# Kernel tuning notes

Hardware: AMD Instinct MI355X
Metric: run time of the kernel (lower is better)

## Reference

```python
import jax, jax.numpy as jnp
import numpy as np
import math

B, D, NH, HD, FF, P, IMG = 4, 768, 12, 64, 3072, 16, 256
L = (IMG // P) ** 2      # 256 tokens
PD = P * P * 3           # 768 patch dim
GRID = IMG // P          # 16


def setup_inputs() -> dict:
    key = jax.random.key(0)
    ks = iter(jax.random.split(key, 80))
    def nrm(shape, s=0.02):
        return jax.random.normal(next(ks), shape, jnp.float32) * s
    return {
        "x": jax.random.normal(next(ks), (B, 3, IMG, IMG), jnp.float32),
        "pe_norm_w": jnp.ones((PD,), jnp.float32),
        "pe_proj_w": nrm((PD, D)),
        "pe_proj_b": jnp.zeros((D,), jnp.float32),
        "pe_norm_out_w": jnp.ones((D,), jnp.float32),
        "pos_embed": nrm((1, L, D)),
        "in_attn_norm_w": jnp.ones((6, D), jnp.float32),
        "in_qkv_w": nrm((6, D, 3 * D)),
        "in_out_w": nrm((6, D, D)),
        "in_ff_norm_w": jnp.ones((6, D), jnp.float32),
        "in_w1": nrm((6, D, 2 * FF)),
        "in_w2": nrm((6, FF, D)),
        "mid_attn_norm_w": jnp.ones((3, D), jnp.float32),
        "mid_qkv_w": nrm((3, D, 3 * D)),
        "mid_out_w": nrm((3, D, D)),
        "mid_ff_norm_w": jnp.ones((3, D), jnp.float32),
        "mid_w1": nrm((3, D, 2 * FF)),
        "mid_w2": nrm((3, FF, D)),
        "out_skip_w": nrm((2 * D, D)),
        "out_skip_b": jnp.zeros((D,), jnp.float32),
        "out_attn_norm_w": jnp.ones((D,), jnp.float32),
        "out_qkv_w": nrm((D, 3 * D)),
        "out_out_w": nrm((D, D)),
        "out_ff_norm_w": jnp.ones((D,), jnp.float32),
        "out_w1": nrm((D, 2 * FF)),
        "out_w2": nrm((FF, D)),
        "final_norm_w": jnp.ones((D,), jnp.float32),
        "ol_proj_w": nrm((D, PD)),
        "ol_proj_b": jnp.zeros((PD,), jnp.float32),
        "rb_conv_in_w": nrm((128, 3, 3, 3), 0.1),
        "rb_gn_w": jnp.ones((5, 128), jnp.float32),
        "rb_gn_b": jnp.zeros((5, 128), jnp.float32),
        "rb_conv1_w": nrm((128, 1, 5, 5), 0.1),
        "rb_conv2_w": nrm((128, 1, 5, 5), 0.1),
        "head_conv_w": nrm((1, 128, 3, 3), 0.1),
    }


def _mish(x):
    return x * jnp.tanh(jax.nn.softplus(x))


def _rms(x, w, eps=1e-5):
    return x * jax.lax.rsqrt(jnp.mean(x * x, axis=-1, keepdims=True) + eps) * w


def _attn(x, qkv_w, out_w):
    b, l, _ = x.shape
    q, k, v = jnp.split(x @ qkv_w, 3, axis=-1)
    s = 1.0 / math.sqrt(HD)  # applied to BOTH q and k, as in source
    q = (q * s).reshape(b, l, NH, HD)
    k = (k * s).reshape(b, l, NH, HD)
    v = v.reshape(b, l, NH, HD)
    logits = jnp.einsum('bqhd,bkhd->bhqk', q, k).astype(jnp.float32)
    w = jax.nn.softmax(logits, axis=-1).astype(x.dtype)
    o = jnp.einsum('bhqk,bkhd->bqhd', w, v).reshape(b, l, NH * HD)
    return o @ out_w


def _ff(x, w1, w2):
    a, g = jnp.split(x @ w1, 2, axis=-1)
    return (_mish(a) * g) @ w2


def _block(x, an, qkv, ow, fn, w1, w2):
    x = x + _attn(_rms(x, an), qkv, ow)
    x = x + _ff(_rms(x, fn), w1, w2)
    return x


def _gn(x, w, b, groups=8, eps=1e-5):
    bb, c, h, ww = x.shape
    xg = x.reshape(bb, groups, c // groups, h, ww)
    m = jnp.mean(xg, axis=(2, 3, 4), keepdims=True)
    v = jnp.var(xg, axis=(2, 3, 4), keepdims=True)
    xn = ((xg - m) * jax.lax.rsqrt(v + eps)).reshape(bb, c, h, ww)
    return xn * w[:, None, None] + b[:, None, None]


def _conv(x, w, pad, dil=1, groups=1):
    xp = jnp.pad(x, ((0, 0), (0, 0), (pad, pad), (pad, pad)), mode='reflect')
    return jax.lax.conv_general_dilated(
        xp, w, window_strides=(1, 1), padding='VALID', rhs_dilation=(dil, dil),
        feature_group_count=groups, dimension_numbers=('NCHW', 'OIHW', 'NCHW'))


def _forward(x, pe_norm_w, pe_proj_w, pe_proj_b, pe_norm_out_w, pos_embed,
             in_attn_norm_w, in_qkv_w, in_out_w, in_ff_norm_w, in_w1, in_w2,
             mid_attn_norm_w, mid_qkv_w, mid_out_w, mid_ff_norm_w, mid_w1, mid_w2,
             out_skip_w, out_skip_b, out_attn_norm_w, out_qkv_w, out_out_w,
             out_ff_norm_w, out_w1, out_w2, final_norm_w, ol_proj_w, ol_proj_b,
             rb_conv_in_w, rb_gn_w, rb_gn_b, rb_conv1_w, rb_conv2_w, head_conv_w):
    b = x.shape[0]
    # PatchEmbed: b c (h p1) (w p2) -> b (h w) (p1 p2 c)
    t = x.reshape(b, 3, GRID, P, GRID, P).transpose(0, 2, 4, 3, 5, 1).reshape(b, L, PD)
    t = _rms(t, pe_norm_w)
    t = t @ pe_proj_w + pe_proj_b
    t = _rms(t, pe_norm_out_w)
    t = t + pos_embed
    # U-ViT trunk: 6 in blocks (skips saved), 3 middle, 1 out block (source typo -> single out block)
    skips = []
    for i in range(6):
        t = _block(t, in_attn_norm_w[i], in_qkv_w[i], in_out_w[i],
                   in_ff_norm_w[i], in_w1[i], in_w2[i])
        skips.append(t)
    for i in range(3):
        t = _block(t, mid_attn_norm_w[i], mid_qkv_w[i], mid_out_w[i],
                   mid_ff_norm_w[i], mid_w1[i], mid_w2[i])
    t = jnp.concatenate([t, skips[-1]], axis=-1) @ out_skip_w + out_skip_b
    t = _block(t, out_attn_norm_w, out_qkv_w, out_out_w, out_ff_norm_w, out_w1, out_w2)
    t = _rms(t, final_norm_w)
    # OutBlock: proj, dropout(eval=identity), unpatchify to b 3 256 256
    t = t @ ol_proj_w + ol_proj_b
    img = t.reshape(b, GRID, GRID, P, P, 3).transpose(0, 5, 1, 3, 2, 4).reshape(b, 3, IMG, IMG)
    # ResNetBlock(128)
    h = _conv(img, rb_conv_in_w, 1)
    h = _mish(_gn(h, rb_gn_w[0], rb_gn_b[0]))
    res = h
    h = _mish(_gn(_conv(h, rb_conv1_w, 2, 1, 128), rb_gn_w[1], rb_gn_b[1]))
    h = res + h
    h = _mish(_gn(h, rb_gn_w[2], rb_gn_b[2]))
    res = h
    h = _mish(_gn(_conv(h, rb_conv2_w, 6, 3, 128), rb_gn_w[3], rb_gn_b[3]))
    h = res + h
    h = _mish(_gn(h, rb_gn_w[4], rb_gn_b[4]))
    return _conv(h, head_conv_w, 1)  # [B, 1, 256, 256]


def reference(x, pe_norm_w, pe_proj_w, pe_proj_b, pe_norm_out_w, pos_embed,
              in_attn_norm_w, in_qkv_w, in_out_w, in_ff_norm_w, in_w1, in_w2,
              mid_attn_norm_w, mid_qkv_w, mid_out_w, mid_ff_norm_w, mid_w1, mid_w2,
              out_skip_w, out_skip_b, out_attn_norm_w, out_qkv_w, out_out_w,
              out_ff_norm_w, out_w1, out_w2, final_norm_w, ol_proj_w, ol_proj_b,
              rb_conv_in_w, rb_gn_w, rb_gn_b, rb_conv1_w, rb_conv2_w, head_conv_w):
    return _forward(x, pe_norm_w, pe_proj_w, pe_proj_b, pe_norm_out_w, pos_embed,
                    in_attn_norm_w, in_qkv_w, in_out_w, in_ff_norm_w, in_w1, in_w2,
                    mid_attn_norm_w, mid_qkv_w, mid_out_w, mid_ff_norm_w, mid_w1, mid_w2,
                    out_skip_w, out_skip_b, out_attn_norm_w, out_qkv_w, out_out_w,
                    out_ff_norm_w, out_w1, out_w2, final_norm_w, ol_proj_w, ol_proj_b,
                    rb_conv_in_w, rb_gn_w, rb_gn_b, rb_conv1_w, rb_conv2_w, head_conv_w)
```

## Files before the change

### kernel.cpp

```cpp
#include <hip/hip_runtime.h>
#include <math.h>

#define B_ 4
#define D_ 768
#define NH_ 12
#define HD_ 64
#define FF_ 3072
#define L_ 256
#define PD_ 768
#define GRID_ 16
#define P_ 16
#define IMG_ 256
#define M_ (B_*L_)
#define NCONV_ (B_*128*IMG_*IMG_)

typedef __attribute__((ext_vector_type(8))) short short8;
typedef __attribute__((ext_vector_type(4))) float f32x4;
typedef __attribute__((ext_vector_type(4))) unsigned short us4;
typedef __attribute__((ext_vector_type(8))) unsigned short us8;
typedef unsigned short ushort_t;

__device__ __forceinline__ float mishf(float x){
    float e = __expf(x);
    float u = (1.f + e) * (1.f + e);
    return x * (1.f - 2.f / (u + 1.f));
}

__device__ __forceinline__ int refl(int i, int n){
    if (i < 0) i = -i;
    if (i >= n) i = 2*n - 2 - i;
    return i;
}

__device__ __forceinline__ ushort_t f2bf(float f){
    unsigned int u = __float_as_uint(f);
    unsigned int r = (u + 0x7FFFu + ((u >> 16) & 1u)) >> 16;
    return (ushort_t)r;
}
__device__ __forceinline__ float bf2f(ushort_t u){
    return __uint_as_float(((unsigned int)u) << 16);
}

__device__ __forceinline__ void block_red2(float& s, float& q){
    #pragma unroll
    for (int o = 32; o > 0; o >>= 1){ s += __shfl_down(s, o); q += __shfl_down(q, o); }
    __shared__ float r1[4], r2[4];
    int tid = threadIdx.x;
    if ((tid & 63) == 0){ r1[tid>>6] = s; r2[tid>>6] = q; }
    __syncthreads();
    if (tid == 0){ s = r1[0]+r1[1]+r1[2]+r1[3]; q = r2[0]+r2[1]+r2[2]+r2[3]; }
    __syncthreads();
}

__global__ __launch_bounds__(256) void k_patchify(const float* __restrict__ x, float* __restrict__ t){
    int idx = blockIdx.x*256 + threadIdx.x;
    int d = idx % PD_; int l = (idx/PD_) % L_; int b = idx/(PD_*L_);
    int c = d % 3; int p = d / 3; int p1 = p / P_; int p2 = p % P_;
    int gh = l / GRID_; int gw = l % GRID_;
    int sy = gh*P_ + p1, sx = gw*P_ + p2;
    t[idx] = x[(((size_t)b*3 + c)*IMG_ + sy)*IMG_ + sx];
}

__global__ __launch_bounds__(256) void k_wt(const float* __restrict__ b0, const float* __restrict__ b1,
                                            const float* __restrict__ b2, int n0, int n1,
                                            ushort_t* __restrict__ dst, int K, int N){
    int z = blockIdx.z;
    size_t sz = (size_t)K * N;
    const float* src = (z < n0) ? b0 + (size_t)z*sz
                     : (z < n0+n1) ? b1 + (size_t)(z-n0)*sz
                     : b2 + (size_t)(z-n0-n1)*sz;
    ushort_t* out = dst + (size_t)z*sz;
    __shared__ float ld[32][33];
    int k0 = blockIdx.y*32, nc0 = blockIdx.x*32;
    int tid = threadIdx.x;
    int c = tid & 31, r8 = tid >> 5;
    #pragma unroll
    for (int i = 0; i < 4; ++i){
        int k = r8 + i*8;
        ld[k][c] = src[(size_t)(k0+k)*N + nc0 + c];
    }
    __syncthreads();
    #pragma unroll
    for (int i = 0; i < 4; ++i){
        int n = r8 + i*8;
        out[(size_t)(nc0+n)*K + k0 + c] = f2bf(ld[c][n]);
    }
}

template<bool OUT_BF>
__global__ __launch_bounds__(256) void k_rms(const float* __restrict__ x, const float* __restrict__ w,
                                             const float* __restrict__ addv, void* __restrict__ yv){
    int row = blockIdx.x;
    const float* xr = x + (size_t)row * D_;
    float s = 0.f;
    for (int i = threadIdx.x; i < D_; i += 256){ float v = xr[i]; s += v*v; }
    __shared__ float red[256];
    red[threadIdx.x] = s; __syncthreads();
    for (int o = 128; o > 0; o >>= 1){
        if (threadIdx.x < o) red[threadIdx.x] += red[threadIdx.x+o];
        __syncthreads();
    }
    float rstd = rsqrtf(red[0]/(float)D_ + 1e-5f);
    int l = row % L_;
    for (int i = threadIdx.x; i < D_; i += 256){
        float v = xr[i]*rstd*w[i];
        if (addv) v += addv[(size_t)l*D_ + i];
        if (OUT_BF) ((ushort_t*)yv)[(size_t)row*D_ + i] = f2bf(v);
        else        ((float*)yv)[(size_t)row*D_ + i] = v;
    }
}

template<bool OBF, int SPLITK>
__global__ __launch_bounds__(256) void k_gemm(const ushort_t* __restrict__ A, const ushort_t* __restrict__ Wt,
                                              void* __restrict__ Cv, const float* __restrict__ bias,
                                              const float* __restrict__ res, int N, int K){
    __shared__ ushort_t As[2][64][40];
    __shared__ ushort_t Ws[2][64][40];
    int tid = threadIdx.x;
    int lane = tid & 63, wid = tid >> 6;
    int wr = wid >> 1, wc = wid & 1;
    int row0 = blockIdx.y * 64, col0 = blockIdx.x * 64;
    f32x4 acc[2][2];
    #pragma unroll
    for (int i = 0; i < 2; ++i)
        #pragma unroll
        for (int j = 0; j < 2; ++j) acc[i][j] = (f32x4){0.f,0.f,0.f,0.f};

    int lg = lane >> 4, lr = lane & 15;
    int sr = tid >> 2, sk = (tid & 3) * 8;
    int kc = K / SPLITK;
    int k0 = (SPLITK > 1) ? blockIdx.z * kc : 0;
    const ushort_t* arow = A  + (size_t)(row0 + sr)*K + k0 + sk;
    const ushort_t* wrow = Wt + (size_t)(col0 + sr)*K + k0 + sk;

    for (int kt = 0; kt < kc; kt += 64){
        __syncthreads();
        *(short8*)&As[0][sr][sk] = *(const short8*)(arow + kt);
        *(short8*)&As[1][sr][sk] = *(const short8*)(arow + kt + 32);
        *(short8*)&Ws[0][sr][sk] = *(const short8*)(wrow + kt);
        *(short8*)&Ws[1][sr][sk] = *(const short8*)(wrow + kt + 32);
        __syncthreads();
        short8 a0[2], a1[2], b0[2], b1[2];
        #pragma unroll
        for (int i = 0; i < 2; ++i){
            a0[i] = *(const short8*)(&As[0][wr*32 + i*16 + lr][lg*8]);
            a1[i] = *(const short8*)(&As[1][wr*32 + i*16 + lr][lg*8]);
        }
        #pragma unroll
        for (int j = 0; j < 2; ++j){
            b0[j] = *(const short8*)(&Ws[0][wc*32 + j*16 + lr][lg*8]);
            b1[j] = *(const short8*)(&Ws[1][wc*32 + j*16 + lr][lg*8]);
        }
        #pragma unroll
        for (int i = 0; i < 2; ++i)
            #pragma unroll
            for (int j = 0; j < 2; ++j){
                acc[i][j] = __builtin_amdgcn_mfma_f32_16x16x32_bf16(a0[i], b0[j], acc[i][j], 0, 0, 0);
                acc[i][j] = __builtin_amdgcn_mfma_f32_16x16x32_bf16(a1[i], b1[j], acc[i][j], 0, 0, 0);
            }
    }
    if (SPLITK > 1){
        float* Pp = (float*)Cv + (size_t)blockIdx.z * M_ * N;
        #pragma unroll
        for (int i = 0; i < 2; ++i)
            #pragma unroll
            for (int j = 0; j < 2; ++j)
                #pragma unroll
                for (int q = 0; q < 4; ++q){
                    int m = row0 + wr*32 + i*16 + lg*4 + q;
                    int n = col0 + wc*32 + j*16 + lr;
                    Pp[(size_t)m*N + n] = acc[i][j][q];
                }
    } else {
        #pragma unroll
        for (int i = 0; i < 2; ++i)
            #pragma unroll
            for (int j = 0; j < 2; ++j)
                #pragma unroll
                for (int q = 0; q < 4; ++q){
                    int m = row0 + wr*32 + i*16 + lg*4 + q;
                    int n = col0 + wc*32 + j*16 + lr;
                    float v = acc[i][j][q];
                    if (bias) v += bias[n];
                    size_t o = (size_t)m*N + n;
                    if (OBF){
                        ((ushort_t*)Cv)[o] = f2bf(v);
                    } else {
                        if (res) v += res[o];
                        ((float*)Cv)[o] = v;
                    }
                }
    }
}

__global__ __launch_bounds__(256) void k_skred(const float* __restrict__ Pp, float* __restrict__ t){
    int idx = blockIdx.x*256 + threadIdx.x;
    size_t e = (size_t)idx*4;
    f32x4 s = *(const f32x4*)(t + e);
    #pragma unroll
    for (int z = 0; z < 4; ++z){
        f32x4 v = *(const f32x4*)(Pp + (size_t)z*M_*D_ + e);
        s.x += v.x; s.y += v.y; s.z += v.z; s.w += v.w;
    }
    *(f32x4*)(t + e) = s;
}

__global__ __launch_bounds__(256) void k_gemm_glu(const ushort_t* __restrict__ A, const ushort_t* __restrict__ Wt,
                                                  ushort_t* __restrict__ Cb, int K){
    __shared__ ushort_t As[2][64][40];
    __shared__ ushort_t Wa[2][64][40];
    __shared__ ushort_t Wg[2][64][40];
    int tid = threadIdx.x;
    int lane = tid & 63, wid = tid >> 6;
    int wr = wid >> 1, wc = wid & 1;
    int row0 = blockIdx.y * 64, col0 = blockIdx.x * 64;
    f32x4 aa[2][2], ag[2][2];
    #pragma unroll
    for (int i = 0; i < 2; ++i)
        #pragma unroll
        for (int j = 0; j < 2; ++j){ aa[i][j] = (f32x4){0.f,0.f,0.f,0.f}; ag[i][j] = (f32x4){0.f,0.f,0.f,0.f}; }

    int lg = lane >> 4, lr = lane & 15;
    int sr = tid >> 2, sk = (tid & 3) * 8;
    const ushort_t* arow = A + (size_t)(row0+sr)*K + sk;
    const ushort_t* war = Wt + (size_t)(col0+sr)*K + sk;
    const ushort_t* wgr = Wt + (size_t)(FF_+col0+sr)*K + sk;

    for (int kt = 0; kt < K; kt += 64){
        __syncthreads();
        *(short8*)&As[0][sr][sk] = *(const short8*)(arow + kt);
        *(short8*)&As[1][sr][sk] = *(const short8*)(arow + kt + 32);
        *(short8*)&Wa[0][sr][sk] = *(const short8*)(war + kt);
        *(short8*)&Wa[1][sr][sk] = *(const short8*)(war + kt + 32);
        *(short8*)&Wg[0][sr][sk] = *(const short8*)(wgr + kt);
        *(short8*)&Wg[1][sr][sk] = *(const short8*)(wgr + kt + 32);
        __syncthreads();
        short8 a0[2], a1[2], ba0[2], ba1[2], bg0[2], bg1[2];
        #pragma unroll
        for (int i = 0; i < 2; ++i){
            a0[i] = *(const short8*)(&As[0][wr*32 + i*16 + lr][lg*8]);
            a1[i] = *(const short8*)(&As[1][wr*32 + i*16 + lr][lg*8]);
        }
        #pragma unroll
        for (int j = 0; j < 2; ++j){
            ba0[j] = *(const short8*)(&Wa[0][wc*32 + j*16 + lr][lg*8]);
            ba1[j] = *(const short8*)(&Wa[1][wc*32 + j*16 + lr][lg*8]);
            bg0[j] = *(const short8*)(&Wg[0][wc*32 + j*16 + lr][lg*8]);
            bg1[j] = *(const short8*)(&Wg[1][wc*32 + j*16 + lr][lg*8]);
        }
        #pragma unroll
        for (int i = 0; i < 2; ++i)
            #pragma unroll
            for (int j = 0; j < 2; ++j){
                aa[i][j] = __builtin_amdgcn_mfma_f32_16x16x32_bf16(a0[i], ba0[j], aa[i][j], 0, 0, 0);
                aa[i][j] = __builtin_amdgcn_mfma_f32_16x16x32_bf16(a1[i], ba1[j], aa[i][j], 0, 0, 0);
                ag[i][j] = __builtin_amdgcn_mfma_f32_16x16x32_bf16(a0[i], bg0[j], ag[i][j], 0, 0, 0);
                ag[i][j] = __builtin_amdgcn_mfma_f32_16x16x32_bf16(a1[i], bg1[j], ag[i][j], 0, 0, 0);
            }
    }
    #pragma unroll
    for (int i = 0; i < 2; ++i)
        #pragma unroll
        for (int j = 0; j < 2; ++j)
            #pragma unroll
            for (int q = 0; q < 4; ++q){
                int m = row0 + wr*32 + i*16 + lg*4 + q;
                int n = col0 + wc*32 + j*16 + lr;
                Cb[(size_t)m*FF_ + n] = f2bf(mishf(aa[i][j][q]) * ag[i][j][q]);
            }
}

__global__ __launch_bounds__(256) void k_attn(const ushort_t* __restrict__ qkv, ushort_t* __restrict__ out){
    int qt = blockIdx.x, h = blockIdx.y, b = blockIdx.z;
    const ushort_t* base = qkv + (size_t)b * L_ * 3 * D_;
    __shared__ ushort_t Qs[64][72];
    __shared__ ushort_t KVs[64][72];
    __shared__ ushort_t Ps[64][268];
    __shared__ float red[8][64];
    int tid = threadIdx.x;
    int lane = tid & 63, w = tid >> 6;
    int lr = lane & 15, lg = lane >> 4;

    {
        int r = tid >> 2, c = (tid & 3) * 16;
        const ushort_t* src = base + (size_t)(qt*64 + r)*3*D_ + h*HD_ + c;
        *(us8*)&Qs[r][c]   = *(const us8*)src;
        *(us8*)&Qs[r][c+8] = *(const us8*)(src + 8);
    }

    f32x4 sacc[4][4];
    #pragma unroll
    for (int kt = 0; kt < 4; ++kt)
        #pragma unroll
        for (int mi = 0; mi < 4; ++mi) sacc[kt][mi] = (f32x4){0.f,0.f,0.f,0.f};

    for (int kt = 0; kt < 4; ++kt){
        __syncthreads();
        {
            int r = tid >> 2, c = (tid & 3) * 16;
            const ushort_t* src = base + (size_t)(kt*64 + r)*3*D_ + D_ + h*HD_ + c;
            *(us8*)&KVs[r][c]   = *(const us8*)src;
            *(us8*)&KVs[r][c+8] = *(const us8*)(src + 8);
        }
        __syncthreads();
        short8 bk0 = *(const short8*)&KVs[w*16 + lr][lg*8];
        short8 bk1 = *(const short8*)&KVs[w*16 + lr][32 + lg*8];
        #pragma unroll
        for (int mi = 0; mi < 4; ++mi){
            short8 a0 = *(const short8*)&Qs[mi*16 + lr][lg*8];
            short8 a1 = *(const short8*)&Qs[mi*16 + lr][32 + lg*8];
            sacc[kt][mi] = __builtin_amdgcn_mfma_f32_16x16x32_bf16(a0, bk0, sacc[kt][mi], 0, 0, 0);
            sacc[kt][mi] = __builtin_amdgcn_mfma_f32_16x16x32_bf16(a1, bk1, sacc[kt][mi], 0, 0, 0);
        }
    }

    const float inv64 = 1.0f/64.0f;
    float gm[4][4], linv[4][4];
    #pragma unroll
    for (int mi = 0; mi < 4; ++mi){
        #pragma unroll
        for (int r = 0; r < 4; ++r){
            float v = fmaxf(fmaxf(sacc[0][mi][r], sacc[1][mi][r]), fmaxf(sacc[2][mi][r], sacc[3][mi][r]));
            v = fmaxf(v, __shfl_xor(v, 1));
            v = fmaxf(v, __shfl_xor(v, 2));
            v = fmaxf(v, __shfl_xor(v, 4));
            v = fmaxf(v, __shfl_xor(v, 8));
            gm[mi][r] = v;
            if (lr == 0) red[w][mi*16 + lg*4 + r] = v;
        }
    }
    __syncthreads();
    #pragma unroll
    for (int mi = 0; mi < 4; ++mi){
        #pragma unroll
        for (int r = 0; r < 4; ++r){
            int row = mi*16 + lg*4 + r;
            float m = fmaxf(fmaxf(red[0][row], red[1][row]), fmaxf(red[2][row], red[3][row]));
            gm[mi][r] = m;
            float sum = 0.f;
            #pragma unroll
            for (int kt = 0; kt < 4; ++kt){
                float p = __expf((sacc[kt][mi][r] - m) * inv64);
                Ps[row][kt*64 + w*16 + lr] = f2bf(p);
                sum += p;
            }
            sum += __shfl_xor(sum, 1);
            sum += __shfl_xor(sum, 2);
            sum += __shfl_xor(sum, 4);
            sum += __shfl_xor(sum, 8);
            linv[mi][r] = sum;
            if (lr == 0) red[4 + w][row] = sum;
        }
    }
    __syncthreads();
    #pragma unroll
    for (int mi = 0; mi < 4; ++mi){
        #pragma unroll
        for (int r = 0; r < 4; ++r){
            int row = mi*16 + lg*4 + r;
            linv[mi][r] = 1.0f / (red[4][row] + red[5][row] + red[6][row] + red[7][row]);
        }
    }

    f32x4 oacc[4];
    #pragma unroll
    for (int mi = 0; mi < 4; ++mi) oacc[mi] = (f32x4){0.f,0.f,0.f,0.f};
    for (int kt = 0; kt < 4; ++kt){
        __syncthreads();
        {
            int k = tid & 63, dg = tid >> 6;
            const ushort_t* src = base + (size_t)(kt*64 + k)*3*D_ + 2*D_ + h*HD_ + dg*16;
            us8 v0 = *(const us8*)src;
            us8 v1 = *(const us8*)(src + 8);
            #pragma unroll
            for (int j = 0; j < 8; ++j) KVs[dg*16 + j][k] = v0[j];
            #pragma unroll
            for (int j = 0; j < 8; ++j) KVs[dg*16 + 8 + j][k] = v1[j];
        }
        __syncthreads();
        short8 bv0 = *(const short8*)&KVs[w*16 + lr][lg*8];
        short8 bv1 = *(const short8*)&KVs[w*16 + lr][32 + lg*8];
        #pragma unroll
        for (int mi = 0; mi < 4; ++mi){
            short8 a0 = *(const short8*)&Ps[mi*16 + lr][kt*64 + lg*8];
            short8 a1 = *(const short8*)&Ps[mi*16 + lr][kt*64 + 32 + lg*8];
            oacc[mi] = __builtin_amdgcn_mfma_f32_16x16x32_bf16(a0, bv0, oacc[mi], 0, 0, 0);
            oacc[mi] = __builtin_amdgcn_mfma_f32_16x16x32_bf16(a1, bv1, oacc[mi], 0, 0, 0);
        }
    }
    #pragma unroll
    for (int mi = 0; mi < 4; ++mi){
        #pragma unroll
        for (int r = 0; r < 4; ++r){
            int row = mi*16 + lg*4 + r;
            out[((size_t)(b*L_ + qt*64 + row))*D_ + h*HD_ + w*16 + lr] = f2bf(oacc[mi][r] * linv[mi][r]);
        }
    }
}

__global__ __launch_bounds__(256) void k_cat(const float* __restrict__ t, const float* __restrict__ skip,
                                             ushort_t* __restrict__ cat){
    int i4 = (blockIdx.x*256 + threadIdx.x) * 4;
    int r = i4 / D_, c = i4 % D_;
    float4 a = *(const float4*)(t + i4);
    float4 b = *(const float4*)(skip + i4);
    us4 ua, ub;
    ua.x=f2bf(a.x); ua.y=f2bf(a.y); ua.z=f2bf(a.z); ua.w=f2bf(a.w);
    ub.x=f2bf(b.x); ub.y=f2bf(b.y); ub.z=f2bf(b.z); ub.w=f2bf(b.w);
    *(us4*)(cat + (size_t)r*1536 + c) = ua;
    *(us4*)(cat + (size_t)r*1536 + 768 + c) = ub;
}

__global__ __launch_bounds__(256) void k_unpatchify(const float* __restrict__ t, float* __restrict__ img){
    int idx = blockIdx.x*256 + threadIdx.x;
    int sx = idx % IMG_; int sy = (idx/IMG_)%IMG_; int c = (idx/(IMG_*IMG_))%3; int b = idx/(3*IMG_*IMG_);
    int gh = sy / P_, p1 = sy % P_, gw = sx / P_, p2 = sx % P_;
    img[idx] = t[(((size_t)b*L_) + gh*GRID_+gw)*PD_ + (p1*P_+p2)*3 + c];
}

__global__ __launch_bounds__(256) void k_conv_in(const float* __restrict__ img, const float* __restrict__ w,
                                                 ushort_t* __restrict__ out, float* __restrict__ partial){
    int y = blockIdx.x, b = blockIdx.y;
    int x = threadIdx.x;
    __shared__ float rows[9][IMG_];
    int yy0 = refl(y-1, IMG_), yy2 = refl(y+1, IMG_);
    #pragma unroll
    for (int ic = 0; ic < 3; ++ic){
        const float* basep = img + ((size_t)(b*3+ic))*IMG_*IMG_;
        rows[ic*3+0][x] = basep[(size_t)yy0*IMG_ + x];
        rows[ic*3+1][x] = basep[(size_t)y  *IMG_ + x];
        rows[ic*3+2][x] = basep[(size_t)yy2*IMG_ + x];
    }
    __syncthreads();
    int xl = (x==0)?1:x-1, xr = (x==255)?254:x+1;
    float sg = 0.f, qg = 0.f;
    for (int oc = 0; oc < 128; ++oc){
        const float* wv = w + oc*27;
        float acc = 0.f;
        #pragma unroll
        for (int ic = 0; ic < 3; ++ic){
            const float* wk = wv + ic*9;
            acc += rows[ic*3+0][xl]*wk[0] + rows[ic*3+0][x]*wk[1] + rows[ic*3+0][xr]*wk[2]
                 + rows[ic*3+1][xl]*wk[3] + rows[ic*3+1][x]*wk[4] + rows[ic*3+1][xr]*wk[5]
                 + rows[ic*3+2][xl]*wk[6] + rows[ic*3+2][x]*wk[7] + rows[ic*3+2][xr]*wk[8];
        }
        out[(((size_t)(b*128+oc))*IMG_ + y)*IMG_ + x] = f2bf(acc);
        sg += acc; qg += acc*acc;
        if ((oc & 15) == 15){
            block_red2(sg, qg);
            if (threadIdx.x == 0){
                int pidx = ((b*8 + (oc>>4))*256 + y);
                partial[pidx*2] = sg; partial[pidx*2+1] = qg;
            }
            sg = 0.f; qg = 0.f;
        }
    }
}

__global__ __launch_bounds__(256) void k_gn_fin(const float* __restrict__ partial, int nper,
                                                float* __restrict__ stats){
    int bg = blockIdx.x, tid = threadIdx.x;
    float s = 0.f, q = 0.f;
    for (int i = tid; i < nper; i += 256){
        s += partial[((size_t)bg*nper + i)*2];
        q += partial[((size_t)bg*nper + i)*2 + 1];
    }
    block_red2(s, q);
    if (tid == 0){
        const float n = 16.f*IMG_*IMG_;
        float m = s/n;
        float var = q/n - m*m;
        stats[bg*2]   = m;
        stats[bg*2+1] = rsqrtf(var + 1e-5f);
    }
}

__global__ __launch_bounds__(256) void k_act(const ushort_t* __restrict__ x, const float* __restrict__ st,
                                             const float* __restrict__ gw, const float* __restrict__ gb,
                                             ushort_t* __restrict__ y){
    int bid = blockIdx.x;
    int b = bid >> 11, c = (bid >> 4) & 127;
    int bg = b*8 + (c>>4);
    float sc = st[bg*2+1]*gw[c], sb = gb[c] - st[bg*2]*sc;
    size_t e0 = (size_t)bid*4096 + threadIdx.x*16;
    us8 v0 = *(const us8*)(x + e0), v1 = *(const us8*)(x + e0 + 8);
    us8 r0, r1;
    #pragma unroll
    for (int i = 0; i < 8; ++i) r0[i] = f2bf(mishf(bf2f(v0[i])*sc + sb));
    #pragma unroll
    for (int i = 0; i < 8; ++i) r1[i] = f2bf(mishf(bf2f(v1[i])*sc + sb));
    *(us8*)(y + e0) = r0;
    *(us8*)(y + e0 + 8) = r1;
}

template<int PAD, int DIL>
__global__ __launch_bounds__(256) void k_dw(const ushort_t* __restrict__ in,
                                            const float* __restrict__ cw,
                                            ushort_t* __restrict__ out, float* __restrict__ partial){
    constexpr int S = 32 + 2*PAD;
    constexpr int SP = (DIL == 1) ? 40 : 52;
    __shared__ float tile[S*SP];
    int tileid = blockIdx.x, c = blockIdx.y, b = blockIdx.z;
    int x0 = (tileid & 7) * 32, y0 = (tileid >> 3) * 32;
    int tid = threadIdx.x;
    const ushort_t* ip = in + ((size_t)(b*128+c))*IMG_*IMG_;
    for (int i = tid; i < S*S; i += 256){
        int r = i / S, cc = i - r*S;
        int gy = refl(y0 - PAD + r, IMG_);
        int gx = refl(x0 - PAD + cc, IMG_);
        tile[r*SP + cc] = bf2f(ip[(size_t)gy*IMG_ + gx]);
    }
    __syncthreads();
    const float* wc = cw + c*25;
    int tx4 = (tid & 7) * 4, ty = tid >> 3;
    float acc[4] = {0.f,0.f,0.f,0.f};
    constexpr int NW = 4*DIL + 4;
    #pragma unroll
    for (int kh = 0; kh < 5; ++kh){
        const float* rowp = &tile[(ty + kh*DIL)*SP + tx4];
        float vv[NW];
        #pragma unroll
        for (int qq = 0; qq < NW/4; ++qq){
            f32x4 v = *(const f32x4*)(rowp + qq*4);
            vv[qq*4+0]=v.x; vv[qq*4+1]=v.y; vv[qq*4+2]=v.z; vv[qq*4+3]=v.w;
        }
        #pragma unroll
        for (int kw = 0; kw < 5; ++kw){
            float wk = wc[kh*5+kw];
            #pragma unroll
            for (int j = 0; j < 4; ++j)
                acc[j] += vv[kw*DIL + j] * wk;
        }
    }
    us4 o4;
    o4.x = f2bf(acc[0]); o4.y = f2bf(acc[1]); o4.z = f2bf(acc[2]); o4.w = f2bf(acc[3]);
    *(us4*)(out + (((size_t)(b*128+c))*IMG_ + y0+ty)*IMG_ + x0+tx4) = o4;
    float s = acc[0]+acc[1]+acc[2]+acc[3];
    float q = acc[0]*acc[0]+acc[1]*acc[1]+acc[2]*acc[2]+acc[3]*acc[3];
    block_red2(s, q);
    if (tid == 0){
        int bid = (b*128 + c)*64 + tileid;
        partial[bid*2] = s; partial[bid*2+1] = q;
    }
}

__global__ __launch_bounds__(256) void k_addmish(const ushort_t* __restrict__ xn, const float* __restrict__ stn,
                                                 const float* __restrict__ wn, const float* __restrict__ bn,
                                                 const ushort_t* __restrict__ resa,
                                                 ushort_t* __restrict__ out, float* __restrict__ partial){
    int bid = blockIdx.x;
    int b = bid >> 11, c = (bid >> 4) & 127;
    int bg = b*8 + (c>>4);
    float scn = stn[bg*2+1]*wn[c], sbn = bn[c] - stn[bg*2]*scn;
    size_t e0 = (size_t)bid*4096 + threadIdx.x*16;
    us8 vn0 = *(const us8*)(xn + e0), vn1 = *(const us8*)(xn + e0 + 8);
    us8 vr0 = *(const us8*)(resa + e0), vr1 = *(const us8*)(resa + e0 + 8);
    us8 r0, r1;
    float s = 0.f, q = 0.f;
    #pragma unroll
    for (int i = 0; i < 8; ++i){
        float v = mishf(bf2f(vn0[i])*scn + sbn) + bf2f(vr0[i]);
        s += v; q += v*v; r0[i] = f2bf(v);
    }
    #pragma unroll
    for (int i = 0; i < 8; ++i){
        float v = mishf(bf2f(vn1[i])*scn + sbn) + bf2f(vr1[i]);
        s += v; q += v*v; r1[i] = f2bf(v);
    }
    *(us8*)(out + e0) = r0;
    *(us8*)(out + e0 + 8) = r1;
    block_red2(s, q);
    if (threadIdx.x == 0){ partial[bid*2] = s; partial[bid*2+1] = q; }
}

__global__ __launch_bounds__(256) void k_head_part(const ushort_t* __restrict__ in, const float* __restrict__ st,
                                                   const float* __restrict__ gw, const float* __restrict__ gb,
                                                   const float* __restrict__ w, float* __restrict__ part){
    __shared__ float tile[34*34];
    int tileid = blockIdx.x, cg = blockIdx.y, b = blockIdx.z;
    int x0 = (tileid & 7)*32, y0 = (tileid >> 3)*32;
    int tid = threadIdx.x;
    int tx4 = (tid & 7)*4, ty = tid >> 3;
    float m  = st[(b*8+cg)*2];
    float rs = st[(b*8+cg)*2 + 1];
    float acc[4] = {0.f,0.f,0.f,0.f};
    for (int ci = 0; ci < 16; ++ci){
        int c = cg*16 + ci;
        float sc = rs*gw[c], sb = gb[c] - m*sc;
        const ushort_t* ip = in + ((size_t)(b*128+c))*IMG_*IMG_;
        if (ci) __syncthreads();
        for (int i = tid; i < 34*34; i += 256){
            int r = i/34, cc = i - r*34;
            int gy = refl(y0-1+r, IMG_);
            int gx = refl(x0-1+cc, IMG_);
            tile[i] = mishf(bf2f(ip[(size_t)gy*IMG_+gx])*sc + sb);
        }
        __syncthreads();
        const float* wc = w + c*9;
        #pragma unroll
        for (int kh = 0; kh < 3; ++kh){
            float vv[6];
            #pragma unroll
            for (int u = 0; u < 6; ++u) vv[u] = tile[(ty+kh)*34 + tx4 + u];
            #pragma unroll
            for (int kw = 0; kw < 3; ++kw){
                float wk = wc[kh*3+kw];
                #pragma unroll
                for (int j = 0; j < 4; ++j) acc[j] += vv[kw+j]*wk;
            }
        }
    }
    f32x4 o = {acc[0], acc[1], acc[2], acc[3]};
    *(f32x4*)(part + (((size_t)(cg*4+b))*IMG_ + y0+ty)*IMG_ + x0+tx4) = o;
}

__global__ __launch_bounds__(256) void k_head_fin(const float* __restrict__ part, float* __restrict__ out){
    int idx4 = blockIdx.x*256 + threadIdx.x;
    size_t e = (size_t)idx4*4;
    int b = (int)(e / (IMG_*IMG_));
    size_t off = e % (IMG_*IMG_);
    f32x4 s = {0.f,0.f,0.f,0.f};
    #pragma unroll
    for (int cg = 0; cg < 8; ++cg){
        f32x4 v = *(const f32x4*)(part + (size_t)(cg*4+b)*IMG_*IMG_ + off);
        s.x += v.x; s.y += v.y; s.z += v.z; s.w += v.w;
    }
    *(f32x4*)(out + e) = s;
}


struct WsMap {
    float *t, *skip, *t2, *ybuf, *img, *partial, *hpart, *stats, *part;
    ushort_t *nb, *qkvb, *ab, *gbuf, *cat, *wb_qkv, *wb_out, *wb_w1, *wb_w2, *wb_pe, *wb_skip, *wb_ol, *cA, *cB;
};

static void run_block(const float* an, const ushort_t* qw, const ushort_t* ow,
                      const float* fn, const ushort_t* w1, const ushort_t* w2,
                      float* t, const WsMap& W, hipStream_t stream){
    k_rms<true><<<M_, 256, 0, stream>>>(t, an, nullptr, W.nb);
    k_gemm<true,1><<<dim3(3*D_/64, M_/64), 256, 0, stream>>>(W.nb, qw, W.qkvb, nullptr, nullptr, 3*D_, D_);
    k_attn<<<dim3(4, NH_, B_), 256, 0, stream>>>(W.qkvb, W.ab);
    k_gemm<false,1><<<dim3(D_/64, M_/64), 256, 0, stream>>>(W.ab, ow, t, nullptr, t, D_, D_);
    k_rms<true><<<M_, 256, 0, stream>>>(t, fn, nullptr, W.nb);
    k_gemm_glu<<<dim3(FF_/64, M_/64), 256, 0, stream>>>(W.nb, w1, W.gbuf, D_);
    k_gemm<false,4><<<dim3(D_/64, M_/64, 4), 256, 0, stream>>>(W.gbuf, w2, W.part, nullptr, nullptr, D_, FF_);
    k_skred<<<(M_*D_)/1024, 256, 0, stream>>>(W.part, t);
}

extern "C" void kernel_launch(void* const* d_in, const int* in_sizes, int n_in,
                              void* d_out, int out_size, void* d_ws, size_t ws_size,
                              hipStream_t stream){
    const float* x              = (const float*)d_in[0];
    const float* pe_norm_w      = (const float*)d_in[1];
    const float* pe_proj_w      = (const float*)d_in[2];
    const float* pe_proj_b      = (const float*)d_in[3];
    const float* pe_norm_out_w  = (const float*)d_in[4];
    const float* pos_embed      = (const float*)d_in[5];
    const float* in_attn_norm_w = (const float*)d_in[6];
    const float* in_qkv_w       = (const float*)d_in[7];
    const float* in_out_w       = (const float*)d_in[8];
    const float* in_ff_norm_w   = (const float*)d_in[9];
    const float* in_w1          = (const float*)d_in[10];
    const float* in_w2          = (const float*)d_in[11];
    const float* mid_attn_norm_w= (const float*)d_in[12];
    const float* mid_qkv_w      = (const float*)d_in[13];
    const float* mid_out_w      = (const float*)d_in[14];
    const float* mid_ff_norm_w  = (const float*)d_in[15];
    const float* mid_w1         = (const float*)d_in[16];
    const float* mid_w2         = (const float*)d_in[17];
    const float* out_skip_w     = (const float*)d_in[18];
    const float* out_skip_b     = (const float*)d_in[19];
    const float* out_attn_norm_w= (const float*)d_in[20];
    const float* out_qkv_w      = (const float*)d_in[21];
    const float* out_out_w      = (const float*)d_in[22];
    const float* out_ff_norm_w  = (const float*)d_in[23];
    const float* out_w1         = (const float*)d_in[24];
    const float* out_w2         = (const float*)d_in[25];
    const float* final_norm_w   = (const float*)d_in[26];
    const float* ol_proj_w      = (const float*)d_in[27];
    const float* ol_proj_b      = (const float*)d_in[28];
    const float* rb_conv_in_w   = (const float*)d_in[29];
    const float* rb_gn_w        = (const float*)d_in[30];
    const float* rb_gn_b        = (const float*)d_in[31];
    const float* rb_conv1_w     = (const float*)d_in[32];
    const float* rb_conv2_w     = (const float*)d_in[33];
    const float* head_conv_w    = (const float*)d_in[34];

    WsMap W;
    float* f = (float*)d_ws;
    const size_t TD = (size_t)M_*D_;
    W.t      = f;               f += TD;
    W.skip   = f;               f += TD;
    W.t2     = f;               f += TD;
    W.ybuf   = f;               f += TD;
    W.img    = f;               f += TD;
    W.partial= f;               f += 131072;
    W.hpart  = f;               f += (size_t)8*4*IMG_*IMG_;
    W.stats  = f;               f += 448;
    W.part   = f;               f += (size_t)4*TD;
    ushort_t* u = (ushort_t*)f;
    W.nb     = u;               u += TD;
    W.qkvb   = u;               u += (size_t)M_*3*D_;
    W.ab     = u;               u += TD;
    W.gbuf   = u;               u += (size_t)M_*FF_;
    W.cat    = u;               u += (size_t)M_*2*D_;
    W.wb_qkv = u;               u += (size_t)10*D_*3*D_;
    W.wb_out = u;               u += (size_t)10*D_*D_;
    W.wb_w1  = u;               u += (size_t)10*D_*2*FF_;
    W.wb_w2  = u;               u += (size_t)10*FF_*D_;
    W.wb_pe  = u;               u += (size_t)D_*D_;
    W.wb_skip= u;               u += (size_t)2*D_*D_;
    W.wb_ol  = u;               u += (size_t)D_*D_;
    W.cA     = u;               u += (size_t)NCONV_;
    W.cB     = u;

    float* st0 = W.stats;       float* st1 = W.stats + 64;
    float* st2 = W.stats + 128; float* st3 = W.stats + 192;
    float* st4 = W.stats + 256;

    k_wt<<<dim3(3*D_/32, D_/32, 10), 256, 0, stream>>>(in_qkv_w, mid_qkv_w, out_qkv_w, 6, 3, W.wb_qkv, D_, 3*D_);
    k_wt<<<dim3(D_/32, D_/32, 10), 256, 0, stream>>>(in_out_w, mid_out_w, out_out_w, 6, 3, W.wb_out, D_, D_);
    k_wt<<<dim3(2*FF_/32, D_/32, 10), 256, 0, stream>>>(in_w1, mid_w1, out_w1, 6, 3, W.wb_w1, D_, 2*FF_);
    k_wt<<<dim3(D_/32, FF_/32, 10), 256, 0, stream>>>(in_w2, mid_w2, out_w2, 6, 3, W.wb_w2, FF_, D_);
    k_wt<<<dim3(D_/32, D_/32, 1), 256, 0, stream>>>(pe_proj_w, nullptr, nullptr, 1, 0, W.wb_pe, D_, D_);
    k_wt<<<dim3(D_/32, 2*D_/32, 1), 256, 0, stream>>>(out_skip_w, nullptr, nullptr, 1, 0, W.wb_skip, 2*D_, D_);
    k_wt<<<dim3(D_/32, D_/32, 1), 256, 0, stream>>>(ol_proj_w, nullptr, nullptr, 1, 0, W.wb_ol, D_, D_);

    k_patchify<<<(B_*L_*PD_)/256, 256, 0, stream>>>(x, W.t2);
    k_rms<true><<<M_, 256, 0, stream>>>(W.t2, pe_norm_w, nullptr, W.nb);
    k_gemm<false,1><<<dim3(D_/64, M_/64), 256, 0, stream>>>(W.nb, W.wb_pe, W.t, pe_proj_b, nullptr, D_, D_);
    k_rms<false><<<M_, 256, 0, stream>>>(W.t, pe_norm_out_w, pos_embed, W.t);

    for (int i = 0; i < 6; ++i){
        run_block(in_attn_norm_w + (size_t)i*D_, W.wb_qkv + (size_t)i*D_*3*D_,
                  W.wb_out + (size_t)i*D_*D_, in_ff_norm_w + (size_t)i*D_,
                  W.wb_w1 + (size_t)i*D_*2*FF_, W.wb_w2 + (size_t)i*FF_*D_,
                  W.t, W, stream);
    }
    hipMemcpyAsync(W.skip, W.t, TD*sizeof(float), hipMemcpyDeviceToDevice, stream);

    for (int i = 0; i < 3; ++i){
        int z = 6 + i;
        run_block(mid_attn_norm_w + (size_t)i*D_, W.wb_qkv + (size_t)z*D_*3*D_,
                  W.wb_out + (size_t)z*D_*D_, mid_ff_norm_w + (size_t)i*D_,
                  W.wb_w1 + (size_t)z*D_*2*FF_, W.wb_w2 + (size_t)z*FF_*D_,
                  W.t, W, stream);
    }

    k_cat<<<(M_*D_)/1024, 256, 0, stream>>>(W.t, W.skip, W.cat);
    k_gemm<false,1><<<dim3(D_/64, M_/64), 256, 0, stream>>>(W.cat, W.wb_skip, W.t2, out_skip_b, nullptr, D_, 2*D_);

    run_block(out_attn_norm_w, W.wb_qkv + (size_t)9*D_*3*D_, W.wb_out + (size_t)9*D_*D_,
              out_ff_norm_w, W.wb_w1 + (size_t)9*D_*2*FF_, W.wb_w2 + (size_t)9*FF_*D_,
              W.t2, W, stream);

    k_rms<true><<<M_, 256, 0, stream>>>(W.t2, final_norm_w, nullptr, W.nb);
    k_gemm<false,1><<<dim3(PD_/64, M_/64), 256, 0, stream>>>(W.nb, W.wb_ol, W.ybuf, ol_proj_b, nullptr, PD_, D_);
    k_unpatchify<<<(B_*3*IMG_*IMG_)/256, 256, 0, stream>>>(W.ybuf, W.img);

    k_conv_in<<<dim3(256, 4), 256, 0, stream>>>(W.img, rb_conv_in_w, W.cA, W.partial);
    k_gn_fin<<<32, 256, 0, stream>>>(W.partial, 256, st0);
    k_act<<<8192, 256, 0, stream>>>(W.cA, st0, rb_gn_w, rb_gn_b, W.cB);
    k_dw<2,1><<<dim3(64, 128, 4), 256, 0, stream>>>(W.cB, rb_conv1_w, W.cA, W.partial);
    k_gn_fin<<<32, 256, 0, stream>>>(W.partial, 1024, st1);
    k_addmish<<<8192, 256, 0, stream>>>(W.cA, st1, rb_gn_w+128, rb_gn_b+128, W.cB, W.cA, W.partial);
    k_gn_fin<<<32, 256, 0, stream>>>(W.partial, 256, st2);
    k_act<<<8192, 256, 0, stream>>>(W.cA, st2, rb_gn_w+256, rb_gn_b+256, W.cB);
    k_dw<6,3><<<dim3(64, 128, 4), 256, 0, stream>>>(W.cB, rb_conv2_w, W.cA, W.partial);
    k_gn_fin<<<32, 256, 0, stream>>>(W.partial, 1024, st3);
    k_addmish<<<8192, 256, 0, stream>>>(W.cA, st3, rb_gn_w+384, rb_gn_b+384, W.cB, W.cA, W.partial);
    k_gn_fin<<<32, 256, 0, stream>>>(W.partial, 256, st4);
    k_head_part<<<dim3(64, 8, 4), 256, 0, stream>>>(W.cA, st4, rb_gn_w+512, rb_gn_b+512, head_conv_w, W.hpart);
    k_head_fin<<<(B_*IMG_*IMG_)/1024, 256, 0, stream>>>(W.hpart, (float*)d_out);
}
```

Measured before the change: 1.550 ms.

## Use 128-row GEMM tiles for QKV/GLU and taller vectorized depthwise conv tiles

Adds a 128x64 tile GEMM for the QKV projection and a 128x32 tile GLU GEMM, so each block reuses its loaded A rows across more MFMAs. The depthwise conv kernel now covers 64 rows per block, loads the tile with vectorized aligned reads when it is away from the image edge, and keeps its weights in registers. The GroupNorm partial counts are halved to match the new tile count. Fewer, larger blocks mean fewer CTAs, so parallelism drops on the small M=1024 GEMMs.

```diff
diff --git a/kernel.cpp b/kernel.cpp
--- a/kernel.cpp
+++ b/kernel.cpp
@@ -193,6 +193,71 @@
     }
 }
 
+template<bool OBF>
+__global__ __launch_bounds__(256) void k_gemmM(const ushort_t* __restrict__ A, const ushort_t* __restrict__ Wt,
+                                               void* __restrict__ Cv, const float* __restrict__ bias,
+                                               const float* __restrict__ res, int N, int K){
+    __shared__ ushort_t As[2][128][40];
+    __shared__ ushort_t Ws[2][64][40];
+    int tid = threadIdx.x;
+    int lane = tid & 63, wid = tid >> 6;
+    int wr = wid >> 1, wc = wid & 1;
+    int row0 = blockIdx.y * 128, col0 = blockIdx.x * 64;
+    f32x4 acc[4][2];
+    #pragma unroll
+    for (int i = 0; i < 4; ++i)
+        #pragma unroll
+        for (int j = 0; j < 2; ++j) acc[i][j] = (f32x4){0.f,0.f,0.f,0.f};
+
+    int lg = lane >> 4, lr = lane & 15;
+    int srA = tid >> 1, ckA = tid & 1;
+    const ushort_t* arow = A + (size_t)(row0 + srA)*K + ckA*32;
+    int srW = tid >> 2, kq = tid & 3;
+    int ckW = kq >> 1, ofW = (kq & 1) * 16;
+    const ushort_t* wrow = Wt + (size_t)(col0 + srW)*K + ckW*32 + ofW;
+
+    for (int kt = 0; kt < K; kt += 64){
+        __syncthreads();
+        #pragma unroll
+        for (int u = 0; u < 4; ++u)
+            *(short8*)&As[ckA][srA][u*8] = *(const short8*)(arow + kt + u*8);
+        *(short8*)&Ws[ckW][srW][ofW]     = *(const short8*)(wrow + kt);
+        *(short8*)&Ws[ckW][srW][ofW + 8] = *(const short8*)(wrow + kt + 8);
+        __syncthreads();
+        #pragma unroll
+        for (int c = 0; c < 2; ++c){
+            short8 a[4], b[2];
+            #pragma unroll
+            for (int i = 0; i < 4; ++i) a[i] = *(const short8*)(&As[c][wr*64 + i*16 + lr][lg*8]);
+            #pragma unroll
+            for (int j = 0; j < 2; ++j) b[j] = *(const short8*)(&Ws[c][wc*32 + j*16 + lr][lg*8]);
+            #pragma unroll
+            for (int i = 0; i < 4; ++i)
+                #pragma unroll
+                for (int j = 0; j < 2; ++j)
+                    acc[i][j] = __builtin_amdgcn_mfma_f32_16x16x32_bf16(a[i], b[j], acc[i][j], 0, 0, 0);
+        }
+    }
+    #pragma unroll
+    for (int i = 0; i < 4; ++i)
+        #pragma unroll
+        for (int j = 0; j < 2; ++j)
+            #pragma unroll
+            for (int q = 0; q < 4; ++q){
+                int m = row0 + wr*64 + i*16 + lg*4 + q;
+                int n = col0 + wc*32 + j*16 + lr;
+                float v = acc[i][j][q];
+                if (bias) v += bias[n];
+                size_t o = (size_t)m*N + n;
+                if (OBF){
+                    ((ushort_t*)Cv)[o] = f2bf(v);
+                } else {
+                    if (res) v += res[o];
+                    ((float*)Cv)[o] = v;
+                }
+            }
+}
+
 __global__ __launch_bounds__(256) void k_skred(const float* __restrict__ Pp, float* __restrict__ t){
     int idx = blockIdx.x*256 + threadIdx.x;
     size_t e = (size_t)idx*4;
@@ -205,69 +270,57 @@
     *(f32x4*)(t + e) = s;
 }
 
-__global__ __launch_bounds__(256) void k_gemm_glu(const ushort_t* __restrict__ A, const ushort_t* __restrict__ Wt,
-                                                  ushort_t* __restrict__ Cb, int K){
-    __shared__ ushort_t As[2][64][40];
-    __shared__ ushort_t Wa[2][64][40];
-    __shared__ ushort_t Wg[2][64][40];
+__global__ __launch_bounds__(256) void k_gemm_gluM(const ushort_t* __restrict__ A, const ushort_t* __restrict__ Wt,
+                                                   ushort_t* __restrict__ Cb, int K){
+    __shared__ ushort_t As[2][128][40];
+    __shared__ ushort_t Wa[2][32][40];
+    __shared__ ushort_t Wg[2][32][40];
     int tid = threadIdx.x;
     int lane = tid & 63, wid = tid >> 6;
     int wr = wid >> 1, wc = wid & 1;
-    int row0 = blockIdx.y * 64, col0 = blockIdx.x * 64;
-    f32x4 aa[2][2], ag[2][2];
-    #pragma unroll
-    for (int i = 0; i < 2; ++i)
-        #pragma unroll
-        for (int j = 0; j < 2; ++j){ aa[i][j] = (f32x4){0.f,0.f,0.f,0.f}; ag[i][j] = (f32x4){0.f,0.f,0.f,0.f}; }
+    int row0 = blockIdx.y * 128, col0 = blockIdx.x * 32;
+    f32x4 aa[4], ag[4];
+    #pragma unroll
+    for (int i = 0; i < 4; ++i){ aa[i] = (f32x4){0.f,0.f,0.f,0.f}; ag[i] = (f32x4){0.f,0.f,0.f,0.f}; }
 
     int lg = lane >> 4, lr = lane & 15;
-    int sr = tid >> 2, sk = (tid & 3) * 8;
-    const ushort_t* arow = A + (size_t)(row0+sr)*K + sk;
-    const ushort_t* war = Wt + (size_t)(col0+sr)*K + sk;
-    const ushort_t* wgr = Wt + (size_t)(FF_+col0+sr)*K + sk;
+    int srA = tid >> 1, ckA = tid & 1;
+    const ushort_t* arow = A + (size_t)(row0 + srA)*K + ckA*32;
+    int srW = tid >> 3, kq = tid & 7;
+    int ckW = kq >> 2, ofW = (kq & 3) * 8;
+    const ushort_t* war = Wt + (size_t)(col0 + srW)*K + ckW*32 + ofW;
+    const ushort_t* wgr = Wt + (size_t)(FF_ + col0 + srW)*K + ckW*32 + ofW;
 
     for (int kt = 0; kt < K; kt += 64){
         __syncthreads();
-        *(short8*)&As[0][sr][sk] = *(const short8*)(arow + kt);
-        *(short8*)&As[1][sr][sk] = *(const short8*)(arow + kt + 32);
-        *(short8*)&Wa[0][sr][sk] = *(const short8*)(war + kt);
-        *(short8*)&Wa[1][sr][sk] = *(const short8*)(war + kt + 32);
-        *(short8*)&Wg[0][sr][sk] = *(const short8*)(wgr + kt);
-        *(short8*)&Wg[1][sr][sk] = *(const short8*)(wgr + kt + 32);
-        __syncthreads();
-        short8 a0[2], a1[2], ba0[2], ba1[2], bg0[2], bg1[2];
-        #pragma unroll
-        for (int i = 0; i < 2; ++i){
-            a0[i] = *(const short8*)(&As[0][wr*32 + i*16 + lr][lg*8]);
-            a1[i] = *(const short8*)(&As[1][wr*32 + i*16 + lr][lg*8]);
-        }
-        #pragma unroll
-        for (int j = 0; j < 2; ++j){
-            ba0[j] = *(const short8*)(&Wa[0][wc*32 + j*16 + lr][lg*8]);
-            ba1[j] = *(const short8*)(&Wa[1][wc*32 + j*16 + lr][lg*8]);
-            bg0[j] = *(const short8*)(&Wg[0][wc*32 + j*16 + lr][lg*8]);
-            bg1[j] = *(const short8*)(&Wg[1][wc*32 + j*16 + lr][lg*8]);
-        }
-        #pragma unroll
-        for (int i = 0; i < 2; ++i)
-            #pragma unroll
-            for (int j = 0; j < 2; ++j){
-                aa[i][j] = __builtin_amdgcn_mfma_f32_16x16x32_bf16(a0[i], ba0[j], aa[i][j], 0, 0, 0);
-                aa[i][j] = __builtin_amdgcn_mfma_f32_16x16x32_bf16(a1[i], ba1[j], aa[i][j], 0, 0, 0);
-                ag[i][j] = __builtin_amdgcn_mfma_f32_16x16x32_bf16(a0[i], bg0[j], ag[i][j], 0, 0, 0);
-                ag[i][j] = __builtin_amdgcn_mfma_f32_16x16x32_bf16(a1[i], bg1[j], ag[i][j], 0, 0, 0);
+        #pragma unroll
+        for (int u = 0; u < 4; ++u)
+            *(short8*)&As[ckA][srA][u*8] = *(const short8*)(arow + kt + u*8);
+        *(short8*)&Wa[ckW][srW][ofW] = *(const short8*)(war + kt);
+        *(short8*)&Wg[ckW][srW][ofW] = *(const short8*)(wgr + kt);
+        __syncthreads();
+        #pragma unroll
+        for (int c = 0; c < 2; ++c){
+            short8 a[4];
+            #pragma unroll
+            for (int i = 0; i < 4; ++i) a[i] = *(const short8*)(&As[c][wr*64 + i*16 + lr][lg*8]);
+            short8 ba = *(const short8*)(&Wa[c][wc*16 + lr][lg*8]);
+            short8 bg = *(const short8*)(&Wg[c][wc*16 + lr][lg*8]);
+            #pragma unroll
+            for (int i = 0; i < 4; ++i){
+                aa[i] = __builtin_amdgcn_mfma_f32_16x16x32_bf16(a[i], ba, aa[i], 0, 0, 0);
+                ag[i] = __builtin_amdgcn_mfma_f32_16x16x32_bf16(a[i], bg, ag[i], 0, 0, 0);
             }
-    }
-    #pragma unroll
-    for (int i = 0; i < 2; ++i)
-        #pragma unroll
-        for (int j = 0; j < 2; ++j)
-            #pragma unroll
-            for (int q = 0; q < 4; ++q){
-                int m = row0 + wr*32 + i*16 + lg*4 + q;
-                int n = col0 + wc*32 + j*16 + lr;
-                Cb[(size_t)m*FF_ + n] = f2bf(mishf(aa[i][j][q]) * ag[i][j][q]);
-            }
+        }
+    }
+    #pragma unroll
+    for (int i = 0; i < 4; ++i)
+        #pragma unroll
+        for (int q = 0; q < 4; ++q){
+            int m = row0 + wr*64 + i*16 + lg*4 + q;
+            int n = col0 + wc*16 + lr;
+            Cb[(size_t)m*FF_ + n] = f2bf(mishf(aa[i][q]) * ag[i][q]);
+        }
 }
 
 __global__ __launch_bounds__(256) void k_attn(const ushort_t* __restrict__ qkv, ushort_t* __restrict__ out){
@@ -497,50 +550,69 @@
 __global__ __launch_bounds__(256) void k_dw(const ushort_t* __restrict__ in,
                                             const float* __restrict__ cw,
                                             ushort_t* __restrict__ out, float* __restrict__ partial){
-    constexpr int S = 32 + 2*PAD;
-    constexpr int SP = (DIL == 1) ? 40 : 52;
-    __shared__ float tile[S*SP];
+    constexpr int AP = (DIL==1) ? 4 : 8;
+    constexpr int SC = (DIL==1) ? 40 : 48;
+    constexpr int SY = 64 + 2*PAD;
+    constexpr int CH = SC/4;
+    __shared__ float tile[SY*SC];
     int tileid = blockIdx.x, c = blockIdx.y, b = blockIdx.z;
-    int x0 = (tileid & 7) * 32, y0 = (tileid >> 3) * 32;
+    int x0 = (tileid & 7) * 32, y0 = (tileid >> 3) * 64;
     int tid = threadIdx.x;
     const ushort_t* ip = in + ((size_t)(b*128+c))*IMG_*IMG_;
-    for (int i = tid; i < S*S; i += 256){
-        int r = i / S, cc = i - r*S;
-        int gy = refl(y0 - PAD + r, IMG_);
-        int gx = refl(x0 - PAD + cc, IMG_);
-        tile[r*SP + cc] = bf2f(ip[(size_t)gy*IMG_ + gx]);
+    int xs = x0 - AP;
+    if (xs >= 0 && xs + SC <= IMG_){
+        for (int j = tid; j < SY*CH; j += 256){
+            int r = j / CH, q = j - r*CH;
+            int gy = refl(y0 - PAD + r, IMG_);
+            us4 v = *(const us4*)(ip + (size_t)gy*IMG_ + xs + q*4);
+            f32x4 fv = { bf2f(v.x), bf2f(v.y), bf2f(v.z), bf2f(v.w) };
+            *(f32x4*)&tile[r*SC + q*4] = fv;
+        }
+    } else {
+        for (int j = tid; j < SY*SC; j += 256){
+            int r = j / SC, cc = j - r*SC;
+            int gy = refl(y0 - PAD + r, IMG_);
+            int gx = refl(xs + cc, IMG_);
+            tile[r*SC + cc] = bf2f(ip[(size_t)gy*IMG_ + gx]);
+        }
     }
     __syncthreads();
-    const float* wc = cw + c*25;
-    int tx4 = (tid & 7) * 4, ty = tid >> 3;
-    float acc[4] = {0.f,0.f,0.f,0.f};
-    constexpr int NW = 4*DIL + 4;
-    #pragma unroll
-    for (int kh = 0; kh < 5; ++kh){
-        const float* rowp = &tile[(ty + kh*DIL)*SP + tx4];
-        float vv[NW];
-        #pragma unroll
-        for (int qq = 0; qq < NW/4; ++qq){
-            f32x4 v = *(const f32x4*)(rowp + qq*4);
-            vv[qq*4+0]=v.x; vv[qq*4+1]=v.y; vv[qq*4+2]=v.z; vv[qq*4+3]=v.w;
-        }
-        #pragma unroll
-        for (int kw = 0; kw < 5; ++kw){
-            float wk = wc[kh*5+kw];
-            #pragma unroll
-            for (int j = 0; j < 4; ++j)
-                acc[j] += vv[kw*DIL + j] * wk;
-        }
-    }
-    us4 o4;
-    o4.x = f2bf(acc[0]); o4.y = f2bf(acc[1]); o4.z = f2bf(acc[2]); o4.w = f2bf(acc[3]);
-    *(us4*)(out + (((size_t)(b*128+c))*IMG_ + y0+ty)*IMG_ + x0+tx4) = o4;
-    float s = acc[0]+acc[1]+acc[2]+acc[3];
-    float q = acc[0]*acc[0]+acc[1]*acc[1]+acc[2]*acc[2]+acc[3]*acc[3];
-    block_red2(s, q);
+    float wreg[25];
+    #pragma unroll
+    for (int u = 0; u < 25; ++u) wreg[u] = cw[c*25 + u];
+    int tx4 = (tid & 7)*4, ty = tid >> 3;
+    constexpr int NV = (DIL==1) ? 3 : 5;
+    float s = 0.f, q2 = 0.f;
+    #pragma unroll
+    for (int rr = 0; rr < 2; ++rr){
+        int yy = ty + rr*32;
+        float acc[4] = {0.f,0.f,0.f,0.f};
+        #pragma unroll
+        for (int kh = 0; kh < 5; ++kh){
+            const float* rowp = &tile[(yy + kh*DIL)*SC + tx4];
+            float vv[NV*4];
+            #pragma unroll
+            for (int u = 0; u < NV; ++u){
+                f32x4 v = *(const f32x4*)(rowp + u*4);
+                vv[u*4]=v.x; vv[u*4+1]=v.y; vv[u*4+2]=v.z; vv[u*4+3]=v.w;
+            }
+            #pragma unroll
+            for (int kw = 0; kw < 5; ++kw){
+                float wk = wreg[kh*5+kw];
+                #pragma unroll
+                for (int j = 0; j < 4; ++j)
+                    acc[j] += vv[kw*DIL + j + (AP - 2*DIL)] * wk;
+            }
+        }
+        us4 o4 = { f2bf(acc[0]), f2bf(acc[1]), f2bf(acc[2]), f2bf(acc[3]) };
+        *(us4*)(out + (((size_t)(b*128+c))*IMG_ + y0+yy)*IMG_ + x0+tx4) = o4;
+        s  += acc[0]+acc[1]+acc[2]+acc[3];
+        q2 += acc[0]*acc[0]+acc[1]*acc[1]+acc[2]*acc[2]+acc[3]*acc[3];
+    }
+    block_red2(s, q2);
     if (tid == 0){
-        int bid = (b*128 + c)*64 + tileid;
-        partial[bid*2] = s; partial[bid*2+1] = q;
+        int bid = (b*128 + c)*32 + tileid;
+        partial[bid*2] = s; partial[bid*2+1] = q2;
     }
 }
 
@@ -638,11 +710,11 @@
                       const float* fn, const ushort_t* w1, const ushort_t* w2,
                       float* t, const WsMap& W, hipStream_t stream){
     k_rms<true><<<M_, 256, 0, stream>>>(t, an, nullptr, W.nb);
-    k_gemm<true,1><<<dim3(3*D_/64, M_/64), 256, 0, stream>>>(W.nb, qw, W.qkvb, nullptr, nullptr, 3*D_, D_);
+    k_gemmM<true><<<dim3(3*D_/64, M_/128), 256, 0, stream>>>(W.nb, qw, W.qkvb, nullptr, nullptr, 3*D_, D_);
     k_attn<<<dim3(4, NH_, B_), 256, 0, stream>>>(W.qkvb, W.ab);
     k_gemm<false,1><<<dim3(D_/64, M_/64), 256, 0, stream>>>(W.ab, ow, t, nullptr, t, D_, D_);
     k_rms<true><<<M_, 256, 0, stream>>>(t, fn, nullptr, W.nb);
-    k_gemm_glu<<<dim3(FF_/64, M_/64), 256, 0, stream>>>(W.nb, w1, W.gbuf, D_);
+    k_gemm_gluM<<<dim3(FF_/32, M_/128), 256, 0, stream>>>(W.nb, w1, W.gbuf, D_);
     k_gemm<false,4><<<dim3(D_/64, M_/64, 4), 256, 0, stream>>>(W.gbuf, w2, W.part, nullptr, nullptr, D_, FF_);
     k_skred<<<(M_*D_)/1024, 256, 0, stream>>>(W.part, t);
 }
@@ -761,13 +833,13 @@
     k_conv_in<<<dim3(256, 4), 256, 0, stream>>>(W.img, rb_conv_in_w, W.cA, W.partial);
     k_gn_fin<<<32, 256, 0, stream>>>(W.partial, 256, st0);
     k_act<<<8192, 256, 0, stream>>>(W.cA, st0, rb_gn_w, rb_gn_b, W.cB);
-    k_dw<2,1><<<dim3(64, 128, 4), 256, 0, stream>>>(W.cB, rb_conv1_w, W.cA, W.partial);
-    k_gn_fin<<<32, 256, 0, stream>>>(W.partial, 1024, st1);
+    k_dw<2,1><<<dim3(32, 128, 4), 256, 0, stream>>>(W.cB, rb_conv1_w, W.cA, W.partial);
+    k_gn_fin<<<32, 256, 0, stream>>>(W.partial, 512, st1);
     k_addmish<<<8192, 256, 0, stream>>>(W.cA, st1, rb_gn_w+128, rb_gn_b+128, W.cB, W.cA, W.partial);
     k_gn_fin<<<32, 256, 0, stream>>>(W.partial, 256, st2);
     k_act<<<8192, 256, 0, stream>>>(W.cA, st2, rb_gn_w+256, rb_gn_b+256, W.cB);
-    k_dw<6,3><<<dim3(64, 128, 4), 256, 0, stream>>>(W.cB, rb_conv2_w, W.cA, W.partial);
-    k_gn_fin<<<32, 256, 0, stream>>>(W.partial, 1024, st3);
+    k_dw<6,3><<<dim3(32, 128, 4), 256, 0, stream>>>(W.cB, rb_conv2_w, W.cA, W.partial);
+    k_gn_fin<<<32, 256, 0, stream>>>(W.partial, 512, st3);
     k_addmish<<<8192, 256, 0, stream>>>(W.cA, st3, rb_gn_w+384, rb_gn_b+384, W.cB, W.cA, W.partial);
     k_gn_fin<<<32, 256, 0, stream>>>(W.partial, 256, st4);
     k_head_part<<<dim3(64, 8, 4), 256, 0, stream>>>(W.cA, st4, rb_gn_w+512, rb_gn_b+512, head_conv_w, W.hpart);
```

Result: no change. 1.559 ms (+0.6%).
